# Kernel optimization log

Hardware: AMD Instinct MI355X
Metric: run time of the kernel (lower is better)

Reference implementation:

```python
import jax, jax.numpy as jnp
import numpy as np

B, P, N, H = 8, 12, 5000, 8
E = 50000
NB = 8
TD0, TD1 = 16, 64
MAX_STEPS = 500


def _proj(x, w1, b1, w2, b2):
    # Projection: Linear -> ReLU -> Linear
    return jax.nn.relu(x @ w1 + b1) @ w2 + b2


def _ln(x, w, b, eps=1e-5):
    # LayerNorm over last two dims [N, H] with affine params [N, H]
    m = jnp.mean(x, axis=(-2, -1), keepdims=True)
    v = jnp.mean((x - m) ** 2, axis=(-2, -1), keepdims=True)
    return (x - m) * jax.lax.rsqrt(v + eps) * w + b


def _time_table():
    # DiffTimeEmbedding buffer: [MAX_STEPS, 2*TD0]
    steps = jnp.arange(MAX_STEPS, dtype=jnp.float32)[:, None]
    dims = jnp.arange(TD0, dtype=jnp.float32)[None, :]
    e = steps * 10.0 ** (dims * 4.0 / TD0)
    return jnp.concatenate([jnp.sin(e), jnp.cos(e)], axis=1)


def setup_inputs() -> dict:
    key = jax.random.key(0)
    ks = jax.random.split(key, 40)
    rn = lambda k, s, sc=0.1: jax.random.normal(k, s, jnp.float32) * sc
    return {
        'x': jax.random.normal(ks[0], (B, P, N), jnp.float32),
        'cond': jax.random.normal(ks[1], (B, P, N, H), jnp.float32),
        'pos': jax.random.normal(ks[2], (N, H), jnp.float32),
        'time': jax.random.randint(ks[3], (B,), 0, MAX_STEPS),
        'edge_index': jax.random.randint(ks[4], (2, E), 0, N),
        'te_w1': rn(ks[5], (2 * TD0, TD1)), 'te_b1': rn(ks[6], (TD1,)),
        'te_w2': rn(ks[7], (TD1, TD1)), 'te_b2': rn(ks[8], (TD1,)),
        'in_w1': rn(ks[9], (1, H)), 'in_b1': rn(ks[10], (H,)),
        'in_w2': rn(ks[11], (H, H)), 'in_b2': rn(ks[12], (H,)),
        'pos_w1': rn(ks[13], (H, H)), 'pos_b1': rn(ks[14], (H,)),
        'pos_w2': rn(ks[15], (H, H)), 'pos_b2': rn(ks[16], (H,)),
        'attn': jax.random.normal(ks[17], (NB + 1, 1), jnp.float32),
        'bt_w1': rn(ks[18], (NB, TD1, H)), 'bt_b1': rn(ks[19], (NB, H)),
        'bt_w2': rn(ks[20], (NB, H, H)), 'bt_b2': rn(ks[21], (NB, H)),
        'bc_w1': rn(ks[22], (NB, H, H)), 'bc_b1': rn(ks[23], (NB, H)),
        'bc_w2': rn(ks[24], (NB, H, H)), 'bc_b2': rn(ks[25], (NB, H)),
        'gn_w': 1.0 + rn(ks[26], (NB, N, H), 0.05), 'gn_b': rn(ks[27], (NB, N, H), 0.05),
        'tn_w': 1.0 + rn(ks[28], (NB, N, H), 0.05), 'tn_b': rn(ks[29], (NB, N, H), 0.05),
        'cv_w': rn(ks[30], (NB, P, P)), 'cv_b': rn(ks[31], (NB, P)),
        'out_w1': rn(ks[32], (H, H)), 'out_b1': rn(ks[33], (H,)),
        'out_w2': rn(ks[34], (H, 1)), 'out_b2': rn(ks[35], (1,)),
    }


def _forward(x, cond, pos, te_w1, te_b1, te_w2, te_b2, in_w1, in_b1, in_w2, in_b2,
             pos_w1, pos_b1, pos_w2, pos_b2, attn, bt_w1, bt_b1, bt_w2, bt_b2,
             bc_w1, bc_b1, bc_w2, bc_b2, gn_w, gn_b, tn_w, tn_b, cv_w, cv_b,
             out_w1, out_b1, out_w2, out_b2, time, edge_index):
    # diffusion-time embedding -> [B, TD1]
    te = _time_table()[time]
    te = jax.nn.silu(te @ te_w1 + te_b1)
    te = jax.nn.silu(te @ te_w2 + te_b2)
    # input + positional projection -> [B, P, N, H]
    h = _proj(x[..., None], in_w1, in_b1, in_w2, in_b2)
    h = h + _proj(pos, pos_w1, pos_b1, pos_w2, pos_b2)
    # LGConv symmetric GCN norm (no self loops), shared across blocks
    src, dst = edge_index[0], edge_index[1]
    deg = jnp.zeros((N,), h.dtype).at[dst].add(1.0)
    dinv = jnp.where(deg > 0, 1.0 / jnp.sqrt(jnp.where(deg > 0, deg, 1.0)), 0.0)
    enorm = dinv[src] * dinv[dst]  # [E]
    skips = [h]
    for i in range(NB):
        t = _proj(te, bt_w1[i], bt_b1[i], bt_w2[i], bt_b2[i])[:, None, None, :]
        c = _proj(cond, bc_w1[i], bc_b1[i], bc_w2[i], bc_b2[i])
        h = _ln(h + c, gn_w[i], gn_b[i])
        # LGConv: gather -> scale -> scatter-add along node dim (-2)
        msg = h[:, :, src, :] * enorm[None, None, :, None]
        h = jnp.zeros_like(h).at[:, :, dst, :].add(msg)
        h = _ln(h + t, tn_w[i], tn_b[i])
        # 1x1 Conv2d over period channels
        h = jnp.einsum('bpnh,qp->bqnh', h, cv_w[i]) + cv_b[i][None, :, None, None]
        skips.append(h)
    s = jnp.stack(skips, axis=-1)  # [B, P, N, H, NB+1]
    a = jax.nn.softmax(attn, axis=0)  # [NB+1, 1]
    h = (s @ a)[..., 0]  # [B, P, N, H]
    return _proj(h, out_w1, out_b1, out_w2, out_b2)[..., 0]  # [B, P, N]


def reference(x, cond, pos, te_w1, te_b1, te_w2, te_b2, in_w1, in_b1, in_w2, in_b2,
              pos_w1, pos_b1, pos_w2, pos_b2, attn, bt_w1, bt_b1, bt_w2, bt_b2,
              bc_w1, bc_b1, bc_w2, bc_b2, gn_w, gn_b, tn_w, tn_b, cv_w, cv_b,
              out_w1, out_b1, out_w2, out_b2, time, edge_index):
    return _forward(x, cond, pos, te_w1, te_b1, te_w2, te_b2, in_w1, in_b1, in_w2, in_b2,
                    pos_w1, pos_b1, pos_w2, pos_b2, attn, bt_w1, bt_b1, bt_w2, bt_b2,
                    bc_w1, bc_b1, bc_w2, bc_b2, gn_w, gn_b, tn_w, tn_b, cv_w, cv_b,
                    out_w1, out_b1, out_w2, out_b2, time, edge_index)
```

## Files before the change

kernel.cpp:

```cpp
#include <hip/hip_runtime.h>
#include <math.h>

#define Bv 8
#define Pv 12
#define Nv 5000
#define Hv 8
#define Ev 50000
#define NBv 8
#define TD1v 64
#define NIMG (Bv * Pv)
#define BLKS_PER_IMG 20
#define ECAP 3072
#define IPT2 2

typedef float f4v __attribute__((ext_vector_type(4)));

__device__ inline float4 nt_load4(const float* p) {
  f4v v = __builtin_nontemporal_load((const f4v*)p);
  return make_float4(v.x, v.y, v.z, v.w);
}
__device__ inline void nt_store4(float* p, float a, float b, float c, float d) {
  f4v v = {a, b, c, d};
  __builtin_nontemporal_store(v, (f4v*)p);
}

__device__ __constant__ float POW10Q[16] = {
  1.0f, 1.7782794100389228f, 3.1622776601683795f, 5.623413251903491f,
  10.0f, 17.78279410038923f, 31.622776601683793f, 56.23413251903491f,
  100.0f, 177.82794100389228f, 316.22776601683796f, 562.341325190349f,
  1000.0f, 1778.2794100389228f, 3162.2776601683795f, 5623.413251903491f
};

__global__ void k_setup(const int* timei, const float* attn,
                        const float* te_w1, const float* te_b1,
                        const float* te_w2, const float* te_b2,
                        const float* bt_w1, const float* bt_b1,
                        const float* bt_w2, const float* bt_b2,
                        float* t_all, float* a9) {
  __shared__ float te0[Bv][32];
  __shared__ float te1[Bv][64];
  __shared__ float te2[Bv][64];
  int t = threadIdx.x;
  for (int idx = t; idx < Bv * 16; idx += 64) {
    int b = idx >> 4, d = idx & 15;
    float e = (float)timei[b] * POW10Q[d];
    te0[b][d]      = (float)sin((double)e);
    te0[b][d + 16] = (float)cos((double)e);
  }
  __syncthreads();
  for (int idx = t; idx < Bv * 64; idx += 64) {
    int b = idx >> 6, j = idx & 63;
    float s = te_b1[j];
    for (int k = 0; k < 32; ++k) s += te0[b][k] * te_w1[k * 64 + j];
    te1[b][j] = s / (1.0f + expf(-s));
  }
  __syncthreads();
  for (int idx = t; idx < Bv * 64; idx += 64) {
    int b = idx >> 6, j = idx & 63;
    float s = te_b2[j];
    for (int k = 0; k < 64; ++k) s += te1[b][k] * te_w2[k * 64 + j];
    te2[b][j] = s / (1.0f + expf(-s));
  }
  __syncthreads();
  {
    int i = t >> 3, b = t & 7;
    float u[Hv];
    for (int j = 0; j < Hv; ++j) {
      float s = bt_b1[i * Hv + j];
      for (int k = 0; k < TD1v; ++k) s += te2[b][k] * bt_w1[(i * TD1v + k) * Hv + j];
      u[j] = fmaxf(s, 0.0f);
    }
    for (int ch = 0; ch < Hv; ++ch) {
      float s = bt_b2[i * Hv + ch];
      for (int j = 0; j < Hv; ++j) s += u[j] * bt_w2[(i * Hv + j) * Hv + ch];
      t_all[(i * Bv + b) * Hv + ch] = s;
    }
  }
  if (t == 0) {
    float m = attn[0];
    for (int i = 1; i < 9; ++i) m = fmaxf(m, attn[i]);
    float s = 0.f, ex[9];
    for (int i = 0; i < 9; ++i) { ex[i] = expf(attn[i] - m); s += ex[i]; }
    for (int i = 0; i < 9; ++i) a9[i] = ex[i] / s;
  }
}

__global__ void k_posp(const float* pos, const float* pw1, const float* pb1,
                       const float* pw2, const float* pb2, float* posp) {
  int n = blockIdx.x * blockDim.x + threadIdx.x;
  if (n >= Nv) return;
  const float4* pr = (const float4*)(pos + (size_t)n * Hv);
  float4 r0 = pr[0], r1 = pr[1];
  float x[8] = {r0.x, r0.y, r0.z, r0.w, r1.x, r1.y, r1.z, r1.w};
  float u[8];
  #pragma unroll
  for (int j = 0; j < 8; ++j) {
    float s = pb1[j];
    #pragma unroll
    for (int k = 0; k < 8; ++k) s += x[k] * pw1[k * 8 + j];
    u[j] = fmaxf(s, 0.f);
  }
  float o[8];
  #pragma unroll
  for (int ch = 0; ch < 8; ++ch) {
    float s = pb2[ch];
    #pragma unroll
    for (int j = 0; j < 8; ++j) s += u[j] * pw2[j * 8 + ch];
    o[ch] = s;
  }
  float4* po = (float4*)(posp + (size_t)n * Hv);
  po[0] = make_float4(o[0], o[1], o[2], o[3]);
  po[1] = make_float4(o[4], o[5], o[6], o[7]);
}

__global__ void k_zero(float* deg, int* cursor, float* stats) {
  int i = blockIdx.x * blockDim.x + threadIdx.x;
  if (i < Nv) { deg[i] = 0.f; cursor[i] = 0; }
  if (i < NBv * 2 * NIMG * 2) stats[i] = 0.f;
}

__global__ void k_deg(const int* eidx, float* deg) {
  int e = blockIdx.x * blockDim.x + threadIdx.x;
  if (e < Ev) atomicAdd(&deg[eidx[Ev + e]], 1.0f);
}

__global__ void k_dinv(const float* deg, float* dinv) {
  int n = blockIdx.x * blockDim.x + threadIdx.x;
  if (n < Nv) {
    float d = deg[n];
    dinv[n] = d > 0.f ? (float)(1.0 / sqrt((double)d)) : 0.f;
  }
}

__global__ void k_scan(const float* deg, int* row_ptr) {
  __shared__ int buf[1024];
  __shared__ int base_s;
  int t = threadIdx.x;
  if (t == 0) { base_s = 0; row_ptr[0] = 0; }
  __syncthreads();
  for (int c = 0; c < 5; ++c) {
    int i = c * 1024 + t;
    int v = (i < Nv) ? (int)(deg[i] + 0.5f) : 0;
    buf[t] = v;
    __syncthreads();
    for (int off = 1; off < 1024; off <<= 1) {
      int add = (t >= off) ? buf[t - off] : 0;
      __syncthreads();
      buf[t] += add;
      __syncthreads();
    }
    int base = base_s;
    if (i < Nv) row_ptr[i + 1] = base + buf[t];
    __syncthreads();
    if (t == 1023) base_s = base + buf[1023];
    __syncthreads();
  }
}

__global__ void k_csr(const int* eidx, const float* dinv, const int* row_ptr,
                      int* cursor, float2* epack) {
  int e = blockIdx.x * blockDim.x + threadIdx.x;
  if (e >= Ev) return;
  int s = eidx[e], d = eidx[Ev + e];
  int slot = atomicAdd(&cursor[d], 1);
  int pos = row_ptr[d] + slot;
  epack[pos] = make_float2(__int_as_float(s), dinv[s] * dinv[d]);
}

__global__ __launch_bounds__(256) void k_gwb(
    const int* __restrict__ row_ptr, const float2* __restrict__ epack,
    const float* __restrict__ gn_w, const float* __restrict__ gn_b,
    float* __restrict__ Gw, float* __restrict__ Gb) {
  int id = blockIdx.x * 256 + threadIdx.x;
  if (id >= NBv * Nv) return;
  int i = id / Nv, n = id % Nv;
  const float* gw = gn_w + (size_t)i * Nv * Hv;
  const float* gb = gn_b + (size_t)i * Nv * Hv;
  float aw[8] = {0,0,0,0,0,0,0,0}, ab[8] = {0,0,0,0,0,0,0,0};
  int e0 = row_ptr[n], e1 = row_ptr[n + 1];
  for (int e = e0; e < e1; ++e) {
    float2 ep = epack[e];
    int s = __float_as_int(ep.x);
    float w = ep.y;
    const float4* wr = (const float4*)(gw + (size_t)s * Hv);
    const float4* br = (const float4*)(gb + (size_t)s * Hv);
    float4 w0 = wr[0], w1 = wr[1], b0 = br[0], b1 = br[1];
    aw[0] += w * w0.x; aw[1] += w * w0.y; aw[2] += w * w0.z; aw[3] += w * w0.w;
    aw[4] += w * w1.x; aw[5] += w * w1.y; aw[6] += w * w1.z; aw[7] += w * w1.w;
    ab[0] += w * b0.x; ab[1] += w * b0.y; ab[2] += w * b0.z; ab[3] += w * b0.w;
    ab[4] += w * b1.x; ab[5] += w * b1.y; ab[6] += w * b1.z; ab[7] += w * b1.w;
  }
  float4* wo = (float4*)(Gw + (size_t)id * Hv);
  wo[0] = make_float4(aw[0], aw[1], aw[2], aw[3]);
  wo[1] = make_float4(aw[4], aw[5], aw[6], aw[7]);
  float4* bo = (float4*)(Gb + (size_t)id * Hv);
  bo[0] = make_float4(ab[0], ab[1], ab[2], ab[3]);
  bo[1] = make_float4(ab[4], ab[5], ab[6], ab[7]);
}

__global__ void k_init(const float* x, const float* posp,
                       const float* iw1, const float* ib1,
                       const float* iw2, const float* ib2,
                       const float* a9, float* hA, float* acc) {
  int t = blockIdx.x * blockDim.x + threadIdx.x;
  if (t >= Bv * Pv * Nv) return;
  float xv = __builtin_nontemporal_load(x + t);
  float u[8];
  #pragma unroll
  for (int j = 0; j < 8; ++j) u[j] = fmaxf(xv * iw1[j] + ib1[j], 0.f);
  int n = t % Nv;
  const float4* pp = (const float4*)(posp + (size_t)n * Hv);
  float4 p0 = pp[0], p1 = pp[1];
  float pv[8] = {p0.x, p0.y, p0.z, p0.w, p1.x, p1.y, p1.z, p1.w};
  float a0 = a9[0];
  float o[8];
  #pragma unroll
  for (int ch = 0; ch < 8; ++ch) {
    float s = ib2[ch];
    #pragma unroll
    for (int j = 0; j < 8; ++j) s += u[j] * iw2[j * 8 + ch];
    o[ch] = s + pv[ch];
  }
  float4* hr = (float4*)(hA + (size_t)t * Hv);
  hr[0] = make_float4(o[0], o[1], o[2], o[3]);
  hr[1] = make_float4(o[4], o[5], o[6], o[7]);
  nt_store4(acc + (size_t)t * Hv,     a0 * o[0], a0 * o[1], a0 * o[2], a0 * o[3]);
  nt_store4(acc + (size_t)t * Hv + 4, a0 * o[4], a0 * o[5], a0 * o[6], a0 * o[7]);
}

__device__ inline void partial_to_stats(float s1, float s2, float* stats_g) {
  #pragma unroll
  for (int off = 32; off > 0; off >>= 1) {
    s1 += __shfl_down(s1, off, 64);
    s2 += __shfl_down(s2, off, 64);
  }
  __shared__ float r1[4], r2[4];
  int wid = threadIdx.x >> 6, lane = threadIdx.x & 63;
  if (lane == 0) { r1[wid] = s1; r2[wid] = s2; }
  __syncthreads();
  if (threadIdx.x == 0) {
    float a = r1[0] + r1[1] + r1[2] + r1[3];
    float b = r2[0] + r2[1] + r2[2] + r2[3];
    atomicAdd(&stats_g[0], a);
    atomicAdd(&stats_g[1], b);
  }
  __syncthreads();
}

__device__ inline void img_swizzle(int bx, int& g, int& chunk) {
  int xcd = bx & 7;
  int local = bx >> 3;
  g = xcd * 12 + local / BLKS_PER_IMG;
  chunk = local % BLKS_PER_IMG;
}

__global__ __launch_bounds__(256) void k_stage1(
    const float* __restrict__ h, const float* __restrict__ cond,
    const float* w1, const float* b1, const float* w2, const float* b2,
    const float* __restrict__ gnw,
    float* __restrict__ vt, float* stats1) {
  __shared__ float lw1[64], lw2[64], lb1[8], lb2[8];
  int t = threadIdx.x;
  if (t < 64) lw1[t] = w1[t];
  else if (t < 128) lw2[t - 64] = w2[t - 64];
  else if (t < 136) lb1[t - 128] = b1[t - 128];
  else if (t < 144) lb2[t - 136] = b2[t - 136];
  __syncthreads();
  int g, chunk;
  img_swizzle(blockIdx.x, g, chunk);
  int n = chunk * 256 + t;
  float s1 = 0.f, s2 = 0.f;
  if (n < Nv) {
    size_t row = ((size_t)g * Nv + n) * Hv;
    float4 c0 = nt_load4(cond + row);
    float4 c1 = nt_load4(cond + row + 4);
    float xc[8] = {c0.x, c0.y, c0.z, c0.w, c1.x, c1.y, c1.z, c1.w};
    float u[8];
    #pragma unroll
    for (int j = 0; j < 8; ++j) {
      float s = lb1[j];
      #pragma unroll
      for (int k = 0; k < 8; ++k) s += xc[k] * lw1[k * 8 + j];
      u[j] = fmaxf(s, 0.f);
    }
    const float4* hr = (const float4*)(h + row);
    float4 h0 = hr[0], h1 = hr[1];
    float hv[8] = {h0.x, h0.y, h0.z, h0.w, h1.x, h1.y, h1.z, h1.w};
    const float4* gr = (const float4*)(gnw + (size_t)n * Hv);
    float4 g0 = gr[0], g1 = gr[1];
    float gv[8] = {g0.x, g0.y, g0.z, g0.w, g1.x, g1.y, g1.z, g1.w};
    float o[8];
    #pragma unroll
    for (int ch = 0; ch < 8; ++ch) {
      float s = lb2[ch];
      #pragma unroll
      for (int j = 0; j < 8; ++j) s += u[j] * lw2[j * 8 + ch];
      float val = s + hv[ch];
      s1 += val; s2 += val * val;
      o[ch] = val * gv[ch];
    }
    float4* vo = (float4*)(vt + row);
    vo[0] = make_float4(o[0], o[1], o[2], o[3]);
    vo[1] = make_float4(o[4], o[5], o[6], o[7]);
  }
  partial_to_stats(s1, s2, stats1 + (size_t)g * 2);
}

__global__ __launch_bounds__(256) void k_stage2(
    const float* __restrict__ vt, float* __restrict__ v2,
    const int* __restrict__ row_ptr, const float2* __restrict__ epack,
    const float* __restrict__ Gw, const float* __restrict__ Gb,
    const float* __restrict__ stats1, float* stats2,
    const float* __restrict__ tvec) {
  __shared__ float2 se[ECAP];
  int t = threadIdx.x;
  int b = blockIdx.x & 7;
  int local = blockIdx.x >> 3;
  int pair = local % 6;
  int chunk = local / 6;
  int g0 = b * Pv + pair * IPT2;
  int nb0 = chunk * 256;
  int nb1 = nb0 + 256; if (nb1 > Nv) nb1 = Nv;
  int eb0 = row_ptr[nb0];
  int eb1 = row_ptr[nb1];
  int cnt = eb1 - eb0;
  const float2* eps;
  int ebase;
  if (cnt <= ECAP) {
    for (int k = t; k < cnt; k += 256) se[k] = epack[eb0 + k];
    eps = se; ebase = eb0;
  } else {
    eps = epack; ebase = 0;
  }
  __syncthreads();
  float mean[IPT2], rstd[IPT2], mrs[IPT2];
  #pragma unroll
  for (int j = 0; j < IPT2; ++j) {
    float m  = stats1[(g0 + j) * 2]     * (1.f / 40000.f);
    float m2 = stats1[(g0 + j) * 2 + 1] * (1.f / 40000.f);
    float var = m2 - m * m;
    mean[j] = m;
    rstd[j] = (float)(1.0 / sqrt((double)var + 1e-5));
    mrs[j]  = m * rstd[j];
  }
  int n = nb0 + t;
  float s1a[IPT2], s2a[IPT2];
  #pragma unroll
  for (int j = 0; j < IPT2; ++j) { s1a[j] = 0.f; s2a[j] = 0.f; }
  if (n < Nv) {
    const float* vt0 = vt + (size_t)(g0 + 0) * Nv * Hv;
    const float* vt1 = vt + (size_t)(g0 + 1) * Nv * Hv;
    float a[IPT2][8];
    #pragma unroll
    for (int j = 0; j < IPT2; ++j)
      #pragma unroll
      for (int ch = 0; ch < 8; ++ch) a[j][ch] = 0.f;
    int e0 = row_ptr[n] - ebase, e1 = row_ptr[n + 1] - ebase;
    int e = e0;
    for (; e + 2 <= e1; e += 2) {
      float2 p0 = eps[e], p1 = eps[e + 1];
      size_t so0 = (size_t)__float_as_int(p0.x) * Hv;
      size_t so1 = (size_t)__float_as_int(p1.x) * Hv;
      const float4* r00 = (const float4*)(vt0 + so0);
      const float4* r01 = (const float4*)(vt1 + so0);
      const float4* r10 = (const float4*)(vt0 + so1);
      const float4* r11 = (const float4*)(vt1 + so1);
      float4 x00a = r00[0], x00b = r00[1];
      float4 x01a = r01[0], x01b = r01[1];
      float4 x10a = r10[0], x10b = r10[1];
      float4 x11a = r11[0], x11b = r11[1];
      a[0][0] += p0.y*x00a.x + p1.y*x10a.x;
      a[0][1] += p0.y*x00a.y + p1.y*x10a.y;
      a[0][2] += p0.y*x00a.z + p1.y*x10a.z;
      a[0][3] += p0.y*x00a.w + p1.y*x10a.w;
      a[0][4] += p0.y*x00b.x + p1.y*x10b.x;
      a[0][5] += p0.y*x00b.y + p1.y*x10b.y;
      a[0][6] += p0.y*x00b.z + p1.y*x10b.z;
      a[0][7] += p0.y*x00b.w + p1.y*x10b.w;
      a[1][0] += p0.y*x01a.x + p1.y*x11a.x;
      a[1][1] += p0.y*x01a.y + p1.y*x11a.y;
      a[1][2] += p0.y*x01a.z + p1.y*x11a.z;
      a[1][3] += p0.y*x01a.w + p1.y*x11a.w;
      a[1][4] += p0.y*x01b.x + p1.y*x11b.x;
      a[1][5] += p0.y*x01b.y + p1.y*x11b.y;
      a[1][6] += p0.y*x01b.z + p1.y*x11b.z;
      a[1][7] += p0.y*x01b.w + p1.y*x11b.w;
    }
    for (; e < e1; ++e) {
      float2 ep = eps[e];
      float w = ep.y;
      size_t so = (size_t)__float_as_int(ep.x) * Hv;
      const float4* r0 = (const float4*)(vt0 + so);
      const float4* r1 = (const float4*)(vt1 + so);
      float4 xa = r0[0], xb = r0[1];
      float4 ya = r1[0], yb = r1[1];
      a[0][0] += w*xa.x; a[0][1] += w*xa.y; a[0][2] += w*xa.z; a[0][3] += w*xa.w;
      a[0][4] += w*xb.x; a[0][5] += w*xb.y; a[0][6] += w*xb.z; a[0][7] += w*xb.w;
      a[1][0] += w*ya.x; a[1][1] += w*ya.y; a[1][2] += w*ya.z; a[1][3] += w*ya.w;
      a[1][4] += w*yb.x; a[1][5] += w*yb.y; a[1][6] += w*yb.z; a[1][7] += w*yb.w;
    }
    size_t noff = (size_t)n * Hv;
    const float4* wr = (const float4*)(Gw + noff);
    const float4* br = (const float4*)(Gb + noff);
    float4 w0 = wr[0], w1 = wr[1], b0 = br[0], b1 = br[1];
    float gw8[8] = {w0.x, w0.y, w0.z, w0.w, w1.x, w1.y, w1.z, w1.w};
    float gb8[8] = {b0.x, b0.y, b0.z, b0.w, b1.x, b1.y, b1.z, b1.w};
    float tl[8];
    {
      const float4* tr = (const float4*)(tvec + b * Hv);
      float4 t0 = tr[0], t1 = tr[1];
      tl[0] = t0.x; tl[1] = t0.y; tl[2] = t0.z; tl[3] = t0.w;
      tl[4] = t1.x; tl[5] = t1.y; tl[6] = t1.z; tl[7] = t1.w;
    }
    #pragma unroll
    for (int j = 0; j < IPT2; ++j) {
      float o[8];
      #pragma unroll
      for (int ch = 0; ch < 8; ++ch) {
        float val = rstd[j] * a[j][ch] - mrs[j] * gw8[ch] + gb8[ch] + tl[ch];
        o[ch] = val;
        s1a[j] += val; s2a[j] += val * val;
      }
      float* vo = v2 + (size_t)(g0 + j) * Nv * Hv + noff;
      nt_store4(vo,     o[0], o[1], o[2], o[3]);
      nt_store4(vo + 4, o[4], o[5], o[6], o[7]);
    }
  }
  #pragma unroll
  for (int j = 0; j < IPT2; ++j)
    partial_to_stats(s1a[j], s2a[j], stats2 + (size_t)(g0 + j) * 2);
}

__global__ __launch_bounds__(256) void k_stage3(
    float* __restrict__ v2, float* __restrict__ acc,
    const float* __restrict__ stats2,
    const float* __restrict__ tnw, const float* __restrict__ tnb,
    const float* __restrict__ cw, const float* __restrict__ cb,
    const float* __restrict__ a9, int iblk) {
  __shared__ float scw[144], scb[12], smean[12], srstd[12];
  int t = threadIdx.x;
  int b = blockIdx.x & 7;
  int chunk = blockIdx.x >> 3;
  if (t < 144) scw[t] = cw[t];
  else if (t < 156) scb[t - 144] = cb[t - 144];
  else if (t < 168) {
    int p = t - 156;
    int g = b * Pv + p;
    float mean = stats2[g * 2]     * (1.f / 40000.f);
    float m2   = stats2[g * 2 + 1] * (1.f / 40000.f);
    float var  = m2 - mean * mean;
    smean[p] = mean;
    srstd[p] = (float)(1.0 / sqrt((double)var + 1e-5));
  }
  __syncthreads();
  int idx = chunk * 256 + t;
  if (idx >= Nv * 2) return;
  int n = idx >> 1, c4 = idx & 1;
  size_t noff = (size_t)n * Hv + c4 * 4;
  const float4 w4 = nt_load4(tnw + noff);
  const float4 b4 = nt_load4(tnb + noff);
  size_t strideP = (size_t)Nv * Hv;
  size_t base = (size_t)b * Pv * strideP + noff;
  float4 in[12];
  #pragma unroll
  for (int p = 0; p < 12; ++p) {
    float4 v = nt_load4(v2 + base + p * strideP);
    float mean = smean[p], rstd = srstd[p];
    in[p].x = (v.x - mean) * rstd * w4.x + b4.x;
    in[p].y = (v.y - mean) * rstd * w4.y + b4.y;
    in[p].z = (v.z - mean) * rstd * w4.z + b4.z;
    in[p].w = (v.w - mean) * rstd * w4.w + b4.w;
  }
  float ai = a9[iblk + 1];
  #pragma unroll
  for (int q = 0; q < 12; ++q) {
    float4 o = make_float4(scb[q], scb[q], scb[q], scb[q]);
    #pragma unroll
    for (int p = 0; p < 12; ++p) {
      float c = scw[q * 12 + p];
      o.x += c * in[p].x; o.y += c * in[p].y;
      o.z += c * in[p].z; o.w += c * in[p].w;
    }
    size_t off = base + q * strideP;
    *(float4*)(v2 + off) = o;
    float4 av = nt_load4(acc + off);
    nt_store4(acc + off, av.x + ai * o.x, av.y + ai * o.y,
                         av.z + ai * o.z, av.w + ai * o.w);
  }
}

__global__ void k_out(const float* acc, const float* ow1, const float* ob1,
                      const float* ow2, const float* ob2, float* out) {
  int t = blockIdx.x * blockDim.x + threadIdx.x;
  if (t >= Bv * Pv * Nv) return;
  float4 a0 = nt_load4(acc + (size_t)t * Hv);
  float4 a1 = nt_load4(acc + (size_t)t * Hv + 4);
  float x[8] = {a0.x, a0.y, a0.z, a0.w, a1.x, a1.y, a1.z, a1.w};
  float o = ob2[0];
  #pragma unroll
  for (int j = 0; j < 8; ++j) {
    float s = ob1[j];
    #pragma unroll
    for (int k = 0; k < 8; ++k) s += x[k] * ow1[k * 8 + j];
    o += fmaxf(s, 0.f) * ow2[j];
  }
  out[t] = o;
}

extern "C" void kernel_launch(void* const* d_in, const int* in_sizes, int n_in,
                              void* d_out, int out_size, void* d_ws, size_t ws_size,
                              hipStream_t stream) {
  const float* x      = (const float*)d_in[0];
  const float* cond   = (const float*)d_in[1];
  const float* pos    = (const float*)d_in[2];
  const int*   timei  = (const int*)  d_in[3];
  const int*   eidx   = (const int*)  d_in[4];
  const float* te_w1  = (const float*)d_in[5];
  const float* te_b1  = (const float*)d_in[6];
  const float* te_w2  = (const float*)d_in[7];
  const float* te_b2  = (const float*)d_in[8];
  const float* in_w1  = (const float*)d_in[9];
  const float* in_b1  = (const float*)d_in[10];
  const float* in_w2  = (const float*)d_in[11];
  const float* in_b2  = (const float*)d_in[12];
  const float* pos_w1 = (const float*)d_in[13];
  const float* pos_b1 = (const float*)d_in[14];
  const float* pos_w2 = (const float*)d_in[15];
  const float* pos_b2 = (const float*)d_in[16];
  const float* attn   = (const float*)d_in[17];
  const float* bt_w1  = (const float*)d_in[18];
  const float* bt_b1  = (const float*)d_in[19];
  const float* bt_w2  = (const float*)d_in[20];
  const float* bt_b2  = (const float*)d_in[21];
  const float* bc_w1  = (const float*)d_in[22];
  const float* bc_b1  = (const float*)d_in[23];
  const float* bc_w2  = (const float*)d_in[24];
  const float* bc_b2  = (const float*)d_in[25];
  const float* gn_w   = (const float*)d_in[26];
  const float* gn_b   = (const float*)d_in[27];
  const float* tn_w   = (const float*)d_in[28];
  const float* tn_b   = (const float*)d_in[29];
  const float* cv_w   = (const float*)d_in[30];
  const float* cv_b   = (const float*)d_in[31];
  const float* out_w1 = (const float*)d_in[32];
  const float* out_b1 = (const float*)d_in[33];
  const float* out_w2 = (const float*)d_in[34];
  const float* out_b2 = (const float*)d_in[35];
  float* out = (float*)d_out;

  const size_t HSZ = (size_t)Bv * Pv * Nv * Hv;
  float* ws    = (float*)d_ws;
  float* X     = ws;
  float* Y     = X + HSZ;
  float* acc   = Y + HSZ;
  float* posp  = acc + HSZ;
  float* deg   = posp + Nv * Hv;
  float* dinv  = deg + Nv;
  float* epack = dinv + Nv;
  float* t_all = epack + 2 * Ev;
  float* a9    = t_all + NBv * Bv * Hv;
  float* stats = a9 + 16;
  float* Gw    = stats + NBv * 2 * NIMG * 2;
  float* Gb    = Gw + NBv * Nv * Hv;
  int* row_ptr = (int*)(Gb + NBv * Nv * Hv);
  int* cursor  = row_ptr + Nv + 8;

  k_setup<<<1, 64, 0, stream>>>(timei, attn, te_w1, te_b1, te_w2, te_b2,
                                bt_w1, bt_b1, bt_w2, bt_b2, t_all, a9);
  k_posp<<<(Nv + 255) / 256, 256, 0, stream>>>(pos, pos_w1, pos_b1, pos_w2, pos_b2, posp);
  k_zero<<<(Nv + 255) / 256, 256, 0, stream>>>(deg, cursor, stats);
  k_deg<<<(Ev + 255) / 256, 256, 0, stream>>>(eidx, deg);
  k_dinv<<<(Nv + 255) / 256, 256, 0, stream>>>(deg, dinv);
  k_scan<<<1, 1024, 0, stream>>>(deg, row_ptr);
  k_csr<<<(Ev + 255) / 256, 256, 0, stream>>>(eidx, dinv, row_ptr, cursor, (float2*)epack);
  k_gwb<<<(NBv * Nv + 255) / 256, 256, 0, stream>>>(
      row_ptr, (const float2*)epack, gn_w, gn_b, Gw, Gb);
  k_init<<<(Bv * Pv * Nv + 255) / 256, 256, 0, stream>>>(
      x, posp, in_w1, in_b1, in_w2, in_b2, a9, X, acc);

  for (int i = 0; i < NBv; ++i) {
    float* st1 = stats + (size_t)(i * 2 + 0) * NIMG * 2;
    float* st2 = stats + (size_t)(i * 2 + 1) * NIMG * 2;
    k_stage1<<<NIMG * BLKS_PER_IMG, 256, 0, stream>>>(
        X, cond,
        bc_w1 + i * 64, bc_b1 + i * 8, bc_w2 + i * 64, bc_b2 + i * 8,
        gn_w + (size_t)i * Nv * Hv,
        Y, st1);
    k_stage2<<<8 * 6 * BLKS_PER_IMG, 256, 0, stream>>>(
        Y, X, row_ptr, (const float2*)epack,
        Gw + (size_t)i * Nv * Hv, Gb + (size_t)i * Nv * Hv,
        st1, st2, t_all + i * Bv * Hv);
    k_stage3<<<8 * 40, 256, 0, stream>>>(
        X, acc, st2,
        tn_w + (size_t)i * Nv * Hv, tn_b + (size_t)i * Nv * Hv,
        cv_w + i * 144, cv_b + i * 12, a9, i);
  }
  k_out<<<(Bv * Pv * Nv + 255) / 256, 256, 0, stream>>>(
      acc, out_w1, out_b1, out_w2, out_b2, out);
}
```

Baseline: 619.8 us.

## Fuse input projection into first stage1 and output projection into last stage3

Removes the separate k_init and k_out kernels. The input projection is recomputed inside the first stage1 pass, which avoids writing the full hidden tensor X and reading it back. The output projection runs in the last stage3 pass, which skips the final acc and v2 stores and uses lane shuffles to assemble the 8-channel row. k_setup is also widened to 512 threads to parallelise the tiny time-embedding MLP. The cost is one more kernel variant and extra register and shared-memory use in the fused kernels.

```diff
diff --git a/kernel.cpp b/kernel.cpp
--- a/kernel.cpp
+++ b/kernel.cpp
@@ -31,50 +31,54 @@
   1000.0f, 1778.2794100389228f, 3162.2776601683795f, 5623.413251903491f
 };
 
-__global__ void k_setup(const int* timei, const float* attn,
-                        const float* te_w1, const float* te_b1,
-                        const float* te_w2, const float* te_b2,
-                        const float* bt_w1, const float* bt_b1,
-                        const float* bt_w2, const float* bt_b2,
-                        float* t_all, float* a9) {
+__global__ __launch_bounds__(512) void k_setup(
+    const int* timei, const float* attn,
+    const float* te_w1, const float* te_b1,
+    const float* te_w2, const float* te_b2,
+    const float* bt_w1, const float* bt_b1,
+    const float* bt_w2, const float* bt_b2,
+    float* t_all, float* a9) {
   __shared__ float te0[Bv][32];
   __shared__ float te1[Bv][64];
   __shared__ float te2[Bv][64];
+  __shared__ float su[64][8];
   int t = threadIdx.x;
-  for (int idx = t; idx < Bv * 16; idx += 64) {
-    int b = idx >> 4, d = idx & 15;
+  if (t < 256) {
+    int b = t >> 5, k = t & 31;
+    int d = k & 15;
     float e = (float)timei[b] * POW10Q[d];
-    te0[b][d]      = (float)sin((double)e);
-    te0[b][d + 16] = (float)cos((double)e);
-  }
-  __syncthreads();
-  for (int idx = t; idx < Bv * 64; idx += 64) {
-    int b = idx >> 6, j = idx & 63;
+    te0[b][k] = (k < 16) ? (float)sin((double)e) : (float)cos((double)e);
+  }
+  __syncthreads();
+  {
+    int b = t >> 6, j = t & 63;
     float s = te_b1[j];
     for (int k = 0; k < 32; ++k) s += te0[b][k] * te_w1[k * 64 + j];
     te1[b][j] = s / (1.0f + expf(-s));
   }
   __syncthreads();
-  for (int idx = t; idx < Bv * 64; idx += 64) {
-    int b = idx >> 6, j = idx & 63;
+  {
+    int b = t >> 6, j = t & 63;
     float s = te_b2[j];
     for (int k = 0; k < 64; ++k) s += te1[b][k] * te_w2[k * 64 + j];
     te2[b][j] = s / (1.0f + expf(-s));
   }
   __syncthreads();
   {
-    int i = t >> 3, b = t & 7;
-    float u[Hv];
-    for (int j = 0; j < Hv; ++j) {
-      float s = bt_b1[i * Hv + j];
-      for (int k = 0; k < TD1v; ++k) s += te2[b][k] * bt_w1[(i * TD1v + k) * Hv + j];
-      u[j] = fmaxf(s, 0.0f);
-    }
-    for (int ch = 0; ch < Hv; ++ch) {
-      float s = bt_b2[i * Hv + ch];
-      for (int j = 0; j < Hv; ++j) s += u[j] * bt_w2[(i * Hv + j) * Hv + ch];
-      t_all[(i * Bv + b) * Hv + ch] = s;
-    }
+    int ib = t >> 3, j = t & 7;
+    int i = ib >> 3, b = ib & 7;
+    float s = bt_b1[i * Hv + j];
+    for (int k = 0; k < TD1v; ++k) s += te2[b][k] * bt_w1[(i * TD1v + k) * Hv + j];
+    su[ib][j] = fmaxf(s, 0.0f);
+  }
+  __syncthreads();
+  {
+    int ib = t >> 3, ch = t & 7;
+    int i = ib >> 3, b = ib & 7;
+    float s = bt_b2[i * Hv + ch];
+    #pragma unroll
+    for (int j = 0; j < 8; ++j) s += su[ib][j] * bt_w2[(i * Hv + j) * Hv + ch];
+    t_all[(i * Bv + b) * Hv + ch] = s;
   }
   if (t == 0) {
     float m = attn[0];
@@ -198,36 +202,6 @@
   bo[1] = make_float4(ab[4], ab[5], ab[6], ab[7]);
 }
 
-__global__ void k_init(const float* x, const float* posp,
-                       const float* iw1, const float* ib1,
-                       const float* iw2, const float* ib2,
-                       const float* a9, float* hA, float* acc) {
-  int t = blockIdx.x * blockDim.x + threadIdx.x;
-  if (t >= Bv * Pv * Nv) return;
-  float xv = __builtin_nontemporal_load(x + t);
-  float u[8];
-  #pragma unroll
-  for (int j = 0; j < 8; ++j) u[j] = fmaxf(xv * iw1[j] + ib1[j], 0.f);
-  int n = t % Nv;
-  const float4* pp = (const float4*)(posp + (size_t)n * Hv);
-  float4 p0 = pp[0], p1 = pp[1];
-  float pv[8] = {p0.x, p0.y, p0.z, p0.w, p1.x, p1.y, p1.z, p1.w};
-  float a0 = a9[0];
-  float o[8];
-  #pragma unroll
-  for (int ch = 0; ch < 8; ++ch) {
-    float s = ib2[ch];
-    #pragma unroll
-    for (int j = 0; j < 8; ++j) s += u[j] * iw2[j * 8 + ch];
-    o[ch] = s + pv[ch];
-  }
-  float4* hr = (float4*)(hA + (size_t)t * Hv);
-  hr[0] = make_float4(o[0], o[1], o[2], o[3]);
-  hr[1] = make_float4(o[4], o[5], o[6], o[7]);
-  nt_store4(acc + (size_t)t * Hv,     a0 * o[0], a0 * o[1], a0 * o[2], a0 * o[3]);
-  nt_store4(acc + (size_t)t * Hv + 4, a0 * o[4], a0 * o[5], a0 * o[6], a0 * o[7]);
-}
-
 __device__ inline void partial_to_stats(float s1, float s2, float* stats_g) {
   #pragma unroll
   for (int off = 32; off > 0; off >>= 1) {
@@ -286,6 +260,81 @@
     const float4* hr = (const float4*)(h + row);
     float4 h0 = hr[0], h1 = hr[1];
     float hv[8] = {h0.x, h0.y, h0.z, h0.w, h1.x, h1.y, h1.z, h1.w};
+    const float4* gr = (const float4*)(gnw + (size_t)n * Hv);
+    float4 g0 = gr[0], g1 = gr[1];
+    float gv[8] = {g0.x, g0.y, g0.z, g0.w, g1.x, g1.y, g1.z, g1.w};
+    float o[8];
+    #pragma unroll
+    for (int ch = 0; ch < 8; ++ch) {
+      float s = lb2[ch];
+      #pragma unroll
+      for (int j = 0; j < 8; ++j) s += u[j] * lw2[j * 8 + ch];
+      float val = s + hv[ch];
+      s1 += val; s2 += val * val;
+      o[ch] = val * gv[ch];
+    }
+    float4* vo = (float4*)(vt + row);
+    vo[0] = make_float4(o[0], o[1], o[2], o[3]);
+    vo[1] = make_float4(o[4], o[5], o[6], o[7]);
+  }
+  partial_to_stats(s1, s2, stats1 + (size_t)g * 2);
+}
+
+__global__ __launch_bounds__(256) void k_stage1_init(
+    const float* __restrict__ x, const float* __restrict__ posp,
+    const float* iw1, const float* ib1, const float* iw2, const float* ib2,
+    const float* __restrict__ cond,
+    const float* w1, const float* b1, const float* w2, const float* b2,
+    const float* __restrict__ gnw, const float* __restrict__ a9,
+    float* __restrict__ acc,
+    float* __restrict__ vt, float* stats1) {
+  __shared__ float lw1[64], lw2[64], lb1[8], lb2[8];
+  __shared__ float li1[8], li2[64], lib1[8], lib2[8];
+  int t = threadIdx.x;
+  if (t < 64) lw1[t] = w1[t];
+  else if (t < 128) lw2[t - 64] = w2[t - 64];
+  else if (t < 136) lb1[t - 128] = b1[t - 128];
+  else if (t < 144) lb2[t - 136] = b2[t - 136];
+  else if (t < 152) li1[t - 144] = iw1[t - 144];
+  else if (t < 216) li2[t - 152] = iw2[t - 152];
+  else if (t < 224) lib1[t - 216] = ib1[t - 216];
+  else if (t < 232) lib2[t - 224] = ib2[t - 224];
+  __syncthreads();
+  int g, chunk;
+  img_swizzle(blockIdx.x, g, chunk);
+  int n = chunk * 256 + t;
+  float s1 = 0.f, s2 = 0.f;
+  if (n < Nv) {
+    size_t row = ((size_t)g * Nv + n) * Hv;
+    float xv = __builtin_nontemporal_load(x + (size_t)g * Nv + n);
+    float ui[8];
+    #pragma unroll
+    for (int j = 0; j < 8; ++j) ui[j] = fmaxf(xv * li1[j] + lib1[j], 0.f);
+    const float4* pp = (const float4*)(posp + (size_t)n * Hv);
+    float4 p0 = pp[0], p1 = pp[1];
+    float pv[8] = {p0.x, p0.y, p0.z, p0.w, p1.x, p1.y, p1.z, p1.w};
+    float hv[8];
+    #pragma unroll
+    for (int ch = 0; ch < 8; ++ch) {
+      float s = lib2[ch];
+      #pragma unroll
+      for (int j = 0; j < 8; ++j) s += ui[j] * li2[j * 8 + ch];
+      hv[ch] = s + pv[ch];
+    }
+    float a0 = a9[0];
+    nt_store4(acc + row,     a0 * hv[0], a0 * hv[1], a0 * hv[2], a0 * hv[3]);
+    nt_store4(acc + row + 4, a0 * hv[4], a0 * hv[5], a0 * hv[6], a0 * hv[7]);
+    float4 c0 = nt_load4(cond + row);
+    float4 c1 = nt_load4(cond + row + 4);
+    float xc[8] = {c0.x, c0.y, c0.z, c0.w, c1.x, c1.y, c1.z, c1.w};
+    float u[8];
+    #pragma unroll
+    for (int j = 0; j < 8; ++j) {
+      float s = lb1[j];
+      #pragma unroll
+      for (int k = 0; k < 8; ++k) s += xc[k] * lw1[k * 8 + j];
+      u[j] = fmaxf(s, 0.f);
+    }
     const float4* gr = (const float4*)(gnw + (size_t)n * Hv);
     float4 g0 = gr[0], g1 = gr[1];
     float gv[8] = {g0.x, g0.y, g0.z, g0.w, g1.x, g1.y, g1.z, g1.w};
@@ -436,11 +485,16 @@
     const float* __restrict__ stats2,
     const float* __restrict__ tnw, const float* __restrict__ tnb,
     const float* __restrict__ cw, const float* __restrict__ cb,
-    const float* __restrict__ a9, int iblk) {
+    const float* __restrict__ a9, int iblk,
+    const float* __restrict__ ow1, const float* __restrict__ ob1,
+    const float* __restrict__ ow2, const float* __restrict__ ob2,
+    float* __restrict__ out) {
   __shared__ float scw[144], scb[12], smean[12], srstd[12];
+  __shared__ float sow1[64], sob1[8], sow2[8], sob2[1];
   int t = threadIdx.x;
   int b = blockIdx.x & 7;
   int chunk = blockIdx.x >> 3;
+  bool last = (iblk == NBv - 1);
   if (t < 144) scw[t] = cw[t];
   else if (t < 156) scb[t - 144] = cb[t - 144];
   else if (t < 168) {
@@ -451,6 +505,11 @@
     float var  = m2 - mean * mean;
     smean[p] = mean;
     srstd[p] = (float)(1.0 / sqrt((double)var + 1e-5));
+  } else if (last) {
+    if (t < 232) sow1[t - 168] = ow1[t - 168];
+    else if (t < 240) sob1[t - 232] = ob1[t - 232];
+    else if (t < 248) sow2[t - 240] = ow2[t - 240];
+    else if (t == 248) sob2[0] = ob2[0];
   }
   __syncthreads();
   int idx = chunk * 256 + t;
@@ -482,29 +541,38 @@
       o.z += c * in[p].z; o.w += c * in[p].w;
     }
     size_t off = base + q * strideP;
-    *(float4*)(v2 + off) = o;
     float4 av = nt_load4(acc + off);
-    nt_store4(acc + off, av.x + ai * o.x, av.y + ai * o.y,
-                         av.z + ai * o.z, av.w + ai * o.w);
-  }
-}
-
-__global__ void k_out(const float* acc, const float* ow1, const float* ob1,
-                      const float* ow2, const float* ob2, float* out) {
-  int t = blockIdx.x * blockDim.x + threadIdx.x;
-  if (t >= Bv * Pv * Nv) return;
-  float4 a0 = nt_load4(acc + (size_t)t * Hv);
-  float4 a1 = nt_load4(acc + (size_t)t * Hv + 4);
-  float x[8] = {a0.x, a0.y, a0.z, a0.w, a1.x, a1.y, a1.z, a1.w};
-  float o = ob2[0];
-  #pragma unroll
-  for (int j = 0; j < 8; ++j) {
-    float s = ob1[j];
-    #pragma unroll
-    for (int k = 0; k < 8; ++k) s += x[k] * ow1[k * 8 + j];
-    o += fmaxf(s, 0.f) * ow2[j];
-  }
-  out[t] = o;
+    float n0 = av.x + ai * o.x, n1 = av.y + ai * o.y;
+    float n2 = av.z + ai * o.z, n3 = av.w + ai * o.w;
+    if (!last) {
+      *(float4*)(v2 + off) = o;
+      nt_store4(acc + off, n0, n1, n2, n3);
+    } else {
+      float e0 = __shfl_xor(n0, 1, 64);
+      float e1 = __shfl_xor(n1, 1, 64);
+      float e2 = __shfl_xor(n2, 1, 64);
+      float e3 = __shfl_xor(n3, 1, 64);
+      float a8[8];
+      if (c4 == 0) {
+        a8[0] = n0; a8[1] = n1; a8[2] = n2; a8[3] = n3;
+        a8[4] = e0; a8[5] = e1; a8[6] = e2; a8[7] = e3;
+      } else {
+        a8[0] = e0; a8[1] = e1; a8[2] = e2; a8[3] = e3;
+        a8[4] = n0; a8[5] = n1; a8[6] = n2; a8[7] = n3;
+      }
+      if (c4 == 0) {
+        float oo = sob2[0];
+        #pragma unroll
+        for (int j = 0; j < 8; ++j) {
+          float s = sob1[j];
+          #pragma unroll
+          for (int k = 0; k < 8; ++k) s += a8[k] * sow1[k * 8 + j];
+          oo += fmaxf(s, 0.f) * sow2[j];
+        }
+        out[((size_t)b * Pv + q) * Nv + n] = oo;
+      }
+    }
+  }
 }
 
 extern "C" void kernel_launch(void* const* d_in, const int* in_sizes, int n_in,
@@ -565,8 +633,8 @@
   int* row_ptr = (int*)(Gb + NBv * Nv * Hv);
   int* cursor  = row_ptr + Nv + 8;
 
-  k_setup<<<1, 64, 0, stream>>>(timei, attn, te_w1, te_b1, te_w2, te_b2,
-                                bt_w1, bt_b1, bt_w2, bt_b2, t_all, a9);
+  k_setup<<<1, 512, 0, stream>>>(timei, attn, te_w1, te_b1, te_w2, te_b2,
+                                 bt_w1, bt_b1, bt_w2, bt_b2, t_all, a9);
   k_posp<<<(Nv + 255) / 256, 256, 0, stream>>>(pos, pos_w1, pos_b1, pos_w2, pos_b2, posp);
   k_zero<<<(Nv + 255) / 256, 256, 0, stream>>>(deg, cursor, stats);
   k_deg<<<(Ev + 255) / 256, 256, 0, stream>>>(eidx, deg);
@@ -575,17 +643,22 @@
   k_csr<<<(Ev + 255) / 256, 256, 0, stream>>>(eidx, dinv, row_ptr, cursor, (float2*)epack);
   k_gwb<<<(NBv * Nv + 255) / 256, 256, 0, stream>>>(
       row_ptr, (const float2*)epack, gn_w, gn_b, Gw, Gb);
-  k_init<<<(Bv * Pv * Nv + 255) / 256, 256, 0, stream>>>(
-      x, posp, in_w1, in_b1, in_w2, in_b2, a9, X, acc);
 
   for (int i = 0; i < NBv; ++i) {
     float* st1 = stats + (size_t)(i * 2 + 0) * NIMG * 2;
     float* st2 = stats + (size_t)(i * 2 + 1) * NIMG * 2;
-    k_stage1<<<NIMG * BLKS_PER_IMG, 256, 0, stream>>>(
-        X, cond,
-        bc_w1 + i * 64, bc_b1 + i * 8, bc_w2 + i * 64, bc_b2 + i * 8,
-        gn_w + (size_t)i * Nv * Hv,
-        Y, st1);
+    if (i == 0) {
+      k_stage1_init<<<NIMG * BLKS_PER_IMG, 256, 0, stream>>>(
+          x, posp, in_w1, in_b1, in_w2, in_b2,
+          cond, bc_w1, bc_b1, bc_w2, bc_b2,
+          gn_w, a9, acc, Y, st1);
+    } else {
+      k_stage1<<<NIMG * BLKS_PER_IMG, 256, 0, stream>>>(
+          X, cond,
+          bc_w1 + i * 64, bc_b1 + i * 8, bc_w2 + i * 64, bc_b2 + i * 8,
+          gn_w + (size_t)i * Nv * Hv,
+          Y, st1);
+    }
     k_stage2<<<8 * 6 * BLKS_PER_IMG, 256, 0, stream>>>(
         Y, X, row_ptr, (const float2*)epack,
         Gw + (size_t)i * Nv * Hv, Gb + (size_t)i * Nv * Hv,
@@ -593,8 +666,7 @@
     k_stage3<<<8 * 40, 256, 0, stream>>>(
         X, acc, st2,
         tn_w + (size_t)i * Nv * Hv, tn_b + (size_t)i * Nv * Hv,
-        cv_w + i * 144, cv_b + i * 12, a9, i);
-  }
-  k_out<<<(Bv * Pv * Nv + 255) / 256, 256, 0, stream>>>(
-      acc, out_w1, out_b1, out_w2, out_b2, out);
-}
+        cv_w + i * 144, cv_b + i * 12, a9, i,
+        out_w1, out_b1, out_w2, out_b2, out);
+  }
+}
```

Result: faster. 598.2 us (-3.5%).
